# Kernel tuning notes

Hardware: AMD Instinct MI355X
Metric: run time of the kernel (lower is better)

Reference implementation:

```python
import jax, jax.numpy as jnp
import numpy as np

H = 16  # num_heads
LN_EPS = 1e-5


def setup_inputs() -> dict:
    key = jax.random.key(0)
    ks = jax.random.split(key, 16)
    B, L, E = 4, 1024, 1024
    x = jax.random.normal(ks[0], (B, L, E), dtype=jnp.float32)
    bias = jax.random.normal(ks[1], (B, H, L, L), dtype=jnp.float32)
    mask = jax.random.randint(ks[2], (B, L), 0, 2, dtype=jnp.int32)
    w = lambda k: jax.random.normal(k, (E, E), dtype=jnp.float32) * 0.02
    return {
        "x": x, "bias": bias, "mask": mask,
        "Wq": w(ks[3]), "bq": jnp.zeros((E,), jnp.float32),
        "Wk": w(ks[4]), "bk": jnp.zeros((E,), jnp.float32),
        "Wv": w(ks[5]), "bv": jnp.zeros((E,), jnp.float32),
        "Wo": w(ks[6]), "bo": jnp.zeros((E,), jnp.float32),
        "gamma": jnp.ones((E,), jnp.float32),
        "beta": jnp.zeros((E,), jnp.float32),
        "gate": jax.random.normal(ks[7], (H,), dtype=jnp.float32) * 0.1,
    }


def reference(x, bias, mask, Wq, bq, Wk, bk, Wv, bv, Wo, bo, gamma, beta, gate):
    B, L, E = x.shape
    D = E // H
    scale = 1.0 / jnp.sqrt(jnp.float32(D))
    residual = x
    # LayerNorm
    mu = jnp.mean(x, axis=-1, keepdims=True)
    var = jnp.mean(jnp.square(x - mu), axis=-1, keepdims=True)
    xn = (x - mu) * jax.lax.rsqrt(var + LN_EPS) * gamma + beta

    def proj(W, b):  # [B,L,E] -> [B,H,L,D]
        return (xn @ W.T + b).reshape(B, L, H, D).transpose(0, 2, 1, 3)

    Q, K, V = proj(Wq, bq), proj(Wk, bk), proj(Wv, bv)
    # logits = QK^T/sqrt(D) + alpha_h * bias   -> [B,H,L,L]
    logits = jnp.einsum("bhqd,bhkd->bhqk", Q, K) * scale
    logits = logits + gate[None, :, None, None] * bias
    mf = mask.astype(x.dtype)
    logits = logits + (1.0 - mf)[:, None, None, :] * -10000.0  # key mask
    attn = jax.nn.softmax(logits, axis=-1)
    attn = jnp.nan_to_num(attn) * mf[:, None, :, None]  # query mask
    out = jnp.einsum("bhqk,bhkd->bqhd", attn, V).reshape(B, L, E)
    out = out * mf[..., None]
    return residual + out @ Wo.T + bo
```

## Files before the change

### kernel.cpp

```cpp
#include <hip/hip_runtime.h>
#include <math.h>

typedef unsigned short u16;
typedef __attribute__((ext_vector_type(8))) short bf16x8;
typedef __attribute__((ext_vector_type(4))) float f32x4;

#define MFMA16(a, b, c) __builtin_amdgcn_mfma_f32_16x16x32_bf16(a, b, c, 0, 0, 0)

__device__ __forceinline__ void gld16(const void* g, void* l) {
  __builtin_amdgcn_global_load_lds((const __attribute__((address_space(1))) void*)g,
                                   (__attribute__((address_space(3))) void*)l, 16, 0, 0);
}

__device__ __forceinline__ u16 f2bf(float f) {
  unsigned u = __float_as_uint(f);
  u += 0x7fffu + ((u >> 16) & 1u);
  return (u16)(u >> 16);
}

__global__ __launch_bounds__(256) void k_castw(const float* __restrict__ wq, const float* __restrict__ wk,
                                               const float* __restrict__ wv, const float* __restrict__ wo,
                                               u16* __restrict__ dst) {
  int t = blockIdx.x * 256 + threadIdx.x;
  int which = t >> 18;
  int off = (t & 0x3ffff) << 2;
  const float* src = (which == 0) ? wq : (which == 1) ? wk : (which == 2) ? wv : wo;
  float4 v = *reinterpret_cast<const float4*>(src + off);
  ushort4 o;
  o.x = f2bf(v.x); o.y = f2bf(v.y); o.z = f2bf(v.z); o.w = f2bf(v.w);
  *reinterpret_cast<ushort4*>(dst + ((size_t)which << 20) + off) = o;
}

__global__ __launch_bounds__(256) void k_ln(const float* __restrict__ x, const float* __restrict__ gamma,
                                            const float* __restrict__ beta, u16* __restrict__ xn) {
  const int row = blockIdx.x, tid = threadIdx.x;
  const int lane = tid & 63, w = tid >> 6;
  const float* xr = x + (size_t)row * 1024;
  float4 v = *reinterpret_cast<const float4*>(xr + tid * 4);
  float s = v.x + v.y + v.z + v.w;
  float s2 = v.x * v.x + v.y * v.y + v.z * v.z + v.w * v.w;
  #pragma unroll
  for (int m = 1; m < 64; m <<= 1) { s += __shfl_xor(s, m); s2 += __shfl_xor(s2, m); }
  __shared__ float ps[4], pq[4];
  if (lane == 0) { ps[w] = s; pq[w] = s2; }
  __syncthreads();
  float S = ps[0] + ps[1] + ps[2] + ps[3];
  float S2 = pq[0] + pq[1] + pq[2] + pq[3];
  float mu = S * (1.f / 1024.f);
  float var = S2 * (1.f / 1024.f) - mu * mu;
  float rstd = rsqrtf(var + 1e-5f);
  float4 g = *reinterpret_cast<const float4*>(gamma + tid * 4);
  float4 bt = *reinterpret_cast<const float4*>(beta + tid * 4);
  ushort4 o;
  o.x = f2bf((v.x - mu) * rstd * g.x + bt.x);
  o.y = f2bf((v.y - mu) * rstd * g.y + bt.y);
  o.z = f2bf((v.z - mu) * rstd * g.z + bt.z);
  o.w = f2bf((v.w - mu) * rstd * g.w + bt.w);
  *reinterpret_cast<ushort4*>(xn + (size_t)row * 1024 + tid * 4) = o;
}

__global__ __launch_bounds__(256) void k_gemm_qkv(const u16* __restrict__ xn,
    const u16* __restrict__ wqb, const u16* __restrict__ wkb, const u16* __restrict__ wvb,
    const float* __restrict__ bq, const float* __restrict__ bk, const float* __restrict__ bv,
    u16* __restrict__ qo, u16* __restrict__ ko, u16* __restrict__ vo) {
  __shared__ __align__(16) u16 lA[128 * 32];
  __shared__ __align__(16) u16 lB[128 * 32];
  const int tid = threadIdx.x;
  const int w = tid >> 6, lane = tid & 63;
  const int wr = w >> 1, wc = w & 1;
  const int lane15 = lane & 15, lgrp = lane >> 4;
  const int m0 = blockIdx.y * 128, n0 = blockIdx.x * 128;
  const int z = blockIdx.z;
  const u16* Bt = (z == 0) ? wqb : (z == 1) ? wkb : wvb;

  f32x4 zero = {0.f, 0.f, 0.f, 0.f};
  f32x4 acc[4][4];
  #pragma unroll
  for (int i = 0; i < 4; i++)
    #pragma unroll
    for (int j = 0; j < 4; j++) acc[i][j] = zero;

  const int srow = w * 16 + (lane >> 2);
  const int scol = (lane & 3) * 8;
  for (int kt = 0; kt < 32; kt++) {
    const int k0 = kt * 32;
    #pragma unroll
    for (int c = 0; c < 2; c++) {
      gld16(xn + (size_t)(m0 + c * 64 + srow) * 1024 + k0 + scol, (char*)lA + c * 4096 + w * 1024);
      gld16(Bt + (size_t)(n0 + c * 64 + srow) * 1024 + k0 + scol, (char*)lB + c * 4096 + w * 1024);
    }
    __syncthreads();
    bf16x8 aF[4], bF[4];
    #pragma unroll
    for (int f = 0; f < 4; f++) {
      aF[f] = *reinterpret_cast<const bf16x8*>(&lA[(wr * 64 + f * 16 + lane15) * 32 + lgrp * 8]);
      bF[f] = *reinterpret_cast<const bf16x8*>(&lB[(wc * 64 + f * 16 + lane15) * 32 + lgrp * 8]);
    }
    #pragma unroll
    for (int fm = 0; fm < 4; fm++)
      #pragma unroll
      for (int fn = 0; fn < 4; fn++)
        acc[fm][fn] = MFMA16(aF[fm], bF[fn], acc[fm][fn]);
    __syncthreads();
  }

  const float* bvec = (z == 0) ? bq : (z == 1) ? bk : bv;
  u16* dst = (z == 0) ? qo : (z == 1) ? ko : vo;
  #pragma unroll
  for (int fm = 0; fm < 4; fm++)
    #pragma unroll
    for (int fn = 0; fn < 4; fn++) {
      const int n = n0 + wc * 64 + fn * 16 + lane15;
      const int h = n >> 6, d = n & 63;
      const float bn = bvec[n];
      #pragma unroll
      for (int j = 0; j < 4; j++) {
        const int m = m0 + wr * 64 + fm * 16 + lgrp * 4 + j;
        const int b = m >> 10, lq = m & 1023;
        dst[(((size_t)(b * 16 + h)) * 1024 + lq) * 64 + d] = f2bf(acc[fm][fn][j] + bn);
      }
    }
}

__global__ __launch_bounds__(256) void k_transpose_v(const u16* __restrict__ V, u16* __restrict__ Vt) {
  __shared__ u16 t[64][64];
  const int bh = blockIdx.y, l0 = blockIdx.x * 64;
  const int tid = threadIdx.x;
  const int r = tid >> 2, c0 = (tid & 3) * 16;
  const u16* src = V + ((size_t)bh * 1024 + l0 + r) * 64 + c0;
  __align__(16) u16 tmp[16];
  *reinterpret_cast<uint4*>(tmp) = *reinterpret_cast<const uint4*>(src);
  *reinterpret_cast<uint4*>(tmp + 8) = *reinterpret_cast<const uint4*>(src + 8);
  #pragma unroll
  for (int i = 0; i < 16; i++) t[c0 + i][r] = tmp[i];
  __syncthreads();
  __align__(16) u16 o[16];
  #pragma unroll
  for (int i = 0; i < 16; i++) o[i] = t[r][c0 + i];
  u16* dst = Vt + ((size_t)bh * 64 + r) * 1024 + l0 + c0;
  *reinterpret_cast<uint4*>(dst) = *reinterpret_cast<const uint4*>(o);
  *reinterpret_cast<uint4*>(dst + 8) = *reinterpret_cast<const uint4*>(o + 8);
}

__global__ __launch_bounds__(256) void k_attn(const u16* __restrict__ Q, const u16* __restrict__ K,
    const u16* __restrict__ Vt, const float* __restrict__ bias, const int* __restrict__ mask,
    const float* __restrict__ gate, u16* __restrict__ O) {
  __shared__ __align__(16) u16 lK[32 * 64];
  __shared__ __align__(16) u16 lV[64 * 32];
  __shared__ __align__(16) u16 lP[4 * 16 * 32];
  const int tid = threadIdx.x;
  const int w = tid >> 6, lane = tid & 63;
  const int lane15 = lane & 15, lgrp = lane >> 4;
  const int bh = blockIdx.y;
  const int b = bh >> 4, h = bh & 15;
  const int q0 = blockIdx.x * 64 + w * 16;
  const float gateh = gate[h];
  const int* mb = mask + b * 1024;
  const float* biasq = bias + ((size_t)bh << 20);

  bf16x8 qf[2];
  #pragma unroll
  for (int kk = 0; kk < 2; kk++)
    qf[kk] = *reinterpret_cast<const bf16x8*>(Q + ((size_t)bh * 1024 + q0 + lane15) * 64 + kk * 32 + lgrp * 8);

  f32x4 zero = {0.f, 0.f, 0.f, 0.f};
  float m_i[4], l_i[4];
  f32x4 accO[4];
  #pragma unroll
  for (int j = 0; j < 4; j++) { m_i[j] = -INFINITY; l_i[j] = 0.f; }
  #pragma unroll
  for (int f = 0; f < 4; f++) accO[f] = zero;

  const int krow = tid >> 3, kcol = (tid & 7) * 8;
  const int vrow = tid >> 2, vcol = (tid & 3) * 8;
  const size_t kbase = (size_t)bh * 1024 * 64;
  const size_t vbase = (size_t)bh * 64 * 1024;

  for (int kb = 0; kb < 1024; kb += 32) {
    gld16(K + kbase + (size_t)(kb + krow) * 64 + kcol, (char*)lK + w * 1024);
    gld16(Vt + vbase + (size_t)vrow * 1024 + kb + vcol, (char*)lV + w * 1024);
    __syncthreads();

    f32x4 s[2];
    #pragma unroll
    for (int fn = 0; fn < 2; fn++) {
      bf16x8 kf0 = *reinterpret_cast<const bf16x8*>(&lK[(fn * 16 + lane15) * 64 + lgrp * 8]);
      bf16x8 kf1 = *reinterpret_cast<const bf16x8*>(&lK[(fn * 16 + lane15) * 64 + 32 + lgrp * 8]);
      s[fn] = MFMA16(qf[0], kf0, zero);
      s[fn] = MFMA16(qf[1], kf1, s[fn]);
    }
    int mk[2];
    float pmax[4] = {-INFINITY, -INFINITY, -INFINITY, -INFINITY};
    #pragma unroll
    for (int fn = 0; fn < 2; fn++) {
      const int kg = kb + fn * 16 + lane15;
      mk[fn] = mb[kg];
      #pragma unroll
      for (int j = 0; j < 4; j++) {
        const int qg = q0 + lgrp * 4 + j;
        float lg = s[fn][j] * 0.125f + gateh * biasq[(size_t)qg * 1024 + kg];
        lg = mk[fn] ? lg : -INFINITY;
        s[fn][j] = lg;
        pmax[j] = fmaxf(pmax[j], lg);
      }
    }
    #pragma unroll
    for (int j = 0; j < 4; j++)
      #pragma unroll
      for (int xm = 1; xm < 16; xm <<= 1)
        pmax[j] = fmaxf(pmax[j], __shfl_xor(pmax[j], xm));

    float corr[4], mnew[4], rs[4];
    #pragma unroll
    for (int j = 0; j < 4; j++) {
      mnew[j] = fmaxf(m_i[j], pmax[j]);
      corr[j] = (m_i[j] == -INFINITY) ? 0.f : __expf(m_i[j] - mnew[j]);
      rs[j] = 0.f;
    }
    #pragma unroll
    for (int fn = 0; fn < 2; fn++)
      #pragma unroll
      for (int j = 0; j < 4; j++) {
        float p = mk[fn] ? __expf(s[fn][j] - mnew[j]) : 0.f;
        rs[j] += p;
        lP[w * 512 + (lgrp * 4 + j) * 32 + fn * 16 + lane15] = f2bf(p);
      }
    #pragma unroll
    for (int j = 0; j < 4; j++) {
      #pragma unroll
      for (int xm = 1; xm < 16; xm <<= 1) rs[j] += __shfl_xor(rs[j], xm);
      l_i[j] = l_i[j] * corr[j] + rs[j];
      m_i[j] = mnew[j];
    }
    #pragma unroll
    for (int f = 0; f < 4; f++)
      #pragma unroll
      for (int j = 0; j < 4; j++) accO[f][j] *= corr[j];

    bf16x8 pf = *reinterpret_cast<const bf16x8*>(&lP[w * 512 + lane15 * 32 + lgrp * 8]);
    #pragma unroll
    for (int f = 0; f < 4; f++) {
      bf16x8 vf = *reinterpret_cast<const bf16x8*>(&lV[(f * 16 + lane15) * 32 + lgrp * 8]);
      accO[f] = MFMA16(pf, vf, accO[f]);
    }
    __syncthreads();
  }

  #pragma unroll
  for (int j = 0; j < 4; j++) {
    const int lq = q0 + lgrp * 4 + j;
    const float inv = (l_i[j] > 0.f) ? 1.f / l_i[j] : 0.f;
    const float mfq = mb[lq] ? 1.f : 0.f;
    #pragma unroll
    for (int f = 0; f < 4; f++) {
      const int d = f * 16 + lane15;
      O[(((size_t)(b * 1024 + lq)) * 16 + h) * 64 + d] = f2bf(accO[f][j] * inv * mfq);
    }
  }
}

__global__ __launch_bounds__(256) void k_gemm_out(const u16* __restrict__ A, const u16* __restrict__ Bt,
    const float* __restrict__ bo, const float* __restrict__ x, float* __restrict__ out) {
  __shared__ __align__(16) u16 lA[128 * 32];
  __shared__ __align__(16) u16 lB[128 * 32];
  const int tid = threadIdx.x;
  const int w = tid >> 6, lane = tid & 63;
  const int wr = w >> 1, wc = w & 1;
  const int lane15 = lane & 15, lgrp = lane >> 4;
  const int m0 = blockIdx.y * 128, n0 = blockIdx.x * 128;

  f32x4 zero = {0.f, 0.f, 0.f, 0.f};
  f32x4 acc[4][4];
  #pragma unroll
  for (int i = 0; i < 4; i++)
    #pragma unroll
    for (int j = 0; j < 4; j++) acc[i][j] = zero;

  const int srow = w * 16 + (lane >> 2);
  const int scol = (lane & 3) * 8;
  for (int kt = 0; kt < 32; kt++) {
    const int k0 = kt * 32;
    #pragma unroll
    for (int c = 0; c < 2; c++) {
      gld16(A + (size_t)(m0 + c * 64 + srow) * 1024 + k0 + scol, (char*)lA + c * 4096 + w * 1024);
      gld16(Bt + (size_t)(n0 + c * 64 + srow) * 1024 + k0 + scol, (char*)lB + c * 4096 + w * 1024);
    }
    __syncthreads();
    bf16x8 aF[4], bF[4];
    #pragma unroll
    for (int f = 0; f < 4; f++) {
      aF[f] = *reinterpret_cast<const bf16x8*>(&lA[(wr * 64 + f * 16 + lane15) * 32 + lgrp * 8]);
      bF[f] = *reinterpret_cast<const bf16x8*>(&lB[(wc * 64 + f * 16 + lane15) * 32 + lgrp * 8]);
    }
    #pragma unroll
    for (int fm = 0; fm < 4; fm++)
      #pragma unroll
      for (int fn = 0; fn < 4; fn++)
        acc[fm][fn] = MFMA16(aF[fm], bF[fn], acc[fm][fn]);
    __syncthreads();
  }

  #pragma unroll
  for (int fm = 0; fm < 4; fm++)
    #pragma unroll
    for (int fn = 0; fn < 4; fn++) {
      const int n = n0 + wc * 64 + fn * 16 + lane15;
      const float bn = bo[n];
      #pragma unroll
      for (int j = 0; j < 4; j++) {
        const int m = m0 + wr * 64 + fm * 16 + lgrp * 4 + j;
        out[(size_t)m * 1024 + n] = acc[fm][fn][j] + bn + x[(size_t)m * 1024 + n];
      }
    }
}

extern "C" void kernel_launch(void* const* d_in, const int* in_sizes, int n_in,
                              void* d_out, int out_size, void* d_ws, size_t ws_size,
                              hipStream_t stream) {
  const float* x     = (const float*)d_in[0];
  const float* bias  = (const float*)d_in[1];
  const int*   mask  = (const int*)d_in[2];
  const float* Wq    = (const float*)d_in[3];
  const float* bq    = (const float*)d_in[4];
  const float* Wk    = (const float*)d_in[5];
  const float* bk    = (const float*)d_in[6];
  const float* Wv    = (const float*)d_in[7];
  const float* bv    = (const float*)d_in[8];
  const float* Wo    = (const float*)d_in[9];
  const float* bo    = (const float*)d_in[10];
  const float* gamma = (const float*)d_in[11];
  const float* beta  = (const float*)d_in[12];
  const float* gate  = (const float*)d_in[13];
  float* out = (float*)d_out;

  u16* wsu  = (u16*)d_ws;
  u16* wqb  = wsu;
  u16* wkb  = wqb  + (1u << 20);
  u16* wvb  = wkb  + (1u << 20);
  u16* wob  = wvb  + (1u << 20);
  u16* xnb  = wob  + (1u << 20);
  u16* qb   = xnb  + (4u << 20);
  u16* kbuf = qb   + (4u << 20);
  u16* vb   = kbuf + (4u << 20);
  u16* vtb  = vb   + (4u << 20);
  u16* ob   = vtb  + (4u << 20);

  k_castw<<<4096, 256, 0, stream>>>(Wq, Wk, Wv, Wo, wqb);
  k_ln<<<4096, 256, 0, stream>>>(x, gamma, beta, xnb);
  k_gemm_qkv<<<dim3(8, 32, 3), 256, 0, stream>>>(xnb, wqb, wkb, wvb, bq, bk, bv, qb, kbuf, vb);
  k_transpose_v<<<dim3(16, 64), 256, 0, stream>>>(vb, vtb);
  k_attn<<<dim3(16, 64), 256, 0, stream>>>(qb, kbuf, vtb, bias, mask, gate, ob);
  k_gemm_out<<<dim3(8, 32), 256, 0, stream>>>(ob, wob, bo, x, out);
}
```

Baseline: 578.4 us.

## Restructure attention kernel: double-buffered 64-key tiles, transposed MFMA, swizzled LDS

Rewrites the flash-attention kernel to process 64 keys per iteration with double-buffered K/V tiles in LDS, prefetching the next tile while computing the current one. Operands are swapped in the MFMAs so each lane owns one query row. That makes softmax reductions need only two cross-lane shuffles, and bias and mask are read as float4/int4 vectors along the key dimension. LDS reads use an XOR swizzle to avoid bank conflicts, and the output is stored as packed vectors. The key mask now adds -10000 instead of forcing -inf, matching the reference. This uses more LDS per block, which may lower occupancy.

```diff
diff --git a/kernel.cpp b/kernel.cpp
--- a/kernel.cpp
+++ b/kernel.cpp
@@ -145,117 +145,128 @@
 __global__ __launch_bounds__(256) void k_attn(const u16* __restrict__ Q, const u16* __restrict__ K,
     const u16* __restrict__ Vt, const float* __restrict__ bias, const int* __restrict__ mask,
     const float* __restrict__ gate, u16* __restrict__ O) {
-  __shared__ __align__(16) u16 lK[32 * 64];
-  __shared__ __align__(16) u16 lV[64 * 32];
-  __shared__ __align__(16) u16 lP[4 * 16 * 32];
+  __shared__ __align__(16) u16 lK[2][4096];
+  __shared__ __align__(16) u16 lV[2][4096];
+  __shared__ __align__(16) u16 lP[4][16 * 72];
   const int tid = threadIdx.x;
   const int w = tid >> 6, lane = tid & 63;
-  const int lane15 = lane & 15, lgrp = lane >> 4;
+  const int l15 = lane & 15, lg4 = lane >> 4;
   const int bh = blockIdx.y;
   const int b = bh >> 4, h = bh & 15;
-  const int q0 = blockIdx.x * 64 + w * 16;
+  const int qg = blockIdx.x * 64 + w * 16 + l15;
   const float gateh = gate[h];
   const int* mb = mask + b * 1024;
-  const float* biasq = bias + ((size_t)bh << 20);
-
-  bf16x8 qf[2];
-  #pragma unroll
-  for (int kk = 0; kk < 2; kk++)
-    qf[kk] = *reinterpret_cast<const bf16x8*>(Q + ((size_t)bh * 1024 + q0 + lane15) * 64 + kk * 32 + lgrp * 8);
+  const float* biasr = bias + ((size_t)bh << 20) + (size_t)qg * 1024;
+  const size_t kvbase = (size_t)bh * 65536;
+
+  bf16x8 qf0 = *reinterpret_cast<const bf16x8*>(Q + kvbase + (size_t)qg * 64 + lg4 * 8);
+  bf16x8 qf1 = *reinterpret_cast<const bf16x8*>(Q + kvbase + (size_t)qg * 64 + 32 + lg4 * 8);
 
   f32x4 zero = {0.f, 0.f, 0.f, 0.f};
-  float m_i[4], l_i[4];
+  float m_i = -INFINITY, l_i = 0.f;
   f32x4 accO[4];
   #pragma unroll
-  for (int j = 0; j < 4; j++) { m_i[j] = -INFINITY; l_i[j] = 0.f; }
-  #pragma unroll
   for (int f = 0; f < 4; f++) accO[f] = zero;
 
-  const int krow = tid >> 3, kcol = (tid & 7) * 8;
-  const int vrow = tid >> 2, vcol = (tid & 3) * 8;
-  const size_t kbase = (size_t)bh * 1024 * 64;
-  const size_t vbase = (size_t)bh * 64 * 1024;
-
-  for (int kb = 0; kb < 1024; kb += 32) {
-    gld16(K + kbase + (size_t)(kb + krow) * 64 + kcol, (char*)lK + w * 1024);
-    gld16(Vt + vbase + (size_t)vrow * 1024 + kb + vcol, (char*)lV + w * 1024);
-    __syncthreads();
-
-    f32x4 s[2];
-    #pragma unroll
-    for (int fn = 0; fn < 2; fn++) {
-      bf16x8 kf0 = *reinterpret_cast<const bf16x8*>(&lK[(fn * 16 + lane15) * 64 + lgrp * 8]);
-      bf16x8 kf1 = *reinterpret_cast<const bf16x8*>(&lK[(fn * 16 + lane15) * 64 + 32 + lgrp * 8]);
-      s[fn] = MFMA16(qf[0], kf0, zero);
-      s[fn] = MFMA16(qf[1], kf1, s[fn]);
-    }
-    int mk[2];
-    float pmax[4] = {-INFINITY, -INFINITY, -INFINITY, -INFINITY};
-    #pragma unroll
-    for (int fn = 0; fn < 2; fn++) {
-      const int kg = kb + fn * 16 + lane15;
-      mk[fn] = mb[kg];
+  const int srow = w * 8 + (lane >> 3);
+  const int scol = ((lane & 7) ^ (lane >> 3)) * 8;
+  const int ldst = w * 1024;
+  const int swz = (l15 & 7) << 4;
+
+  #pragma unroll
+  for (int c = 0; c < 2; c++) {
+    gld16(K + kvbase + (size_t)(c * 32 + srow) * 64 + scol, (char*)lK[0] + c * 4096 + ldst);
+    gld16(Vt + kvbase + (size_t)(c * 32 + srow) * 1024 + scol, (char*)lV[0] + c * 4096 + ldst);
+  }
+  __syncthreads();
+
+  int cur = 0;
+  for (int t = 0; t < 16; t++) {
+    const int kb = t * 64;
+    if (t < 15) {
+      const int kb2 = kb + 64;
+      #pragma unroll
+      for (int c = 0; c < 2; c++) {
+        gld16(K + kvbase + (size_t)(kb2 + c * 32 + srow) * 64 + scol, (char*)lK[cur ^ 1] + c * 4096 + ldst);
+        gld16(Vt + kvbase + (size_t)(c * 32 + srow) * 1024 + kb2 + scol, (char*)lV[cur ^ 1] + c * 4096 + ldst);
+      }
+    }
+
+    const char* lkb = (const char*)lK[cur];
+    f32x4 s[4];
+    #pragma unroll
+    for (int fn = 0; fn < 4; fn++) {
+      const char* rowp = lkb + (fn * 16 + l15) * 128;
+      bf16x8 kf0 = *reinterpret_cast<const bf16x8*>(rowp + ((lg4 * 16) ^ swz));
+      bf16x8 kf1 = *reinterpret_cast<const bf16x8*>(rowp + ((64 + lg4 * 16) ^ swz));
+      s[fn] = MFMA16(kf0, qf0, zero);
+      s[fn] = MFMA16(kf1, qf1, s[fn]);
+    }
+
+    float p[16];
+    float pmax = -INFINITY;
+    #pragma unroll
+    for (int fn = 0; fn < 4; fn++) {
+      const int kg = kb + fn * 16 + lg4 * 4;
+      float4 b4 = *reinterpret_cast<const float4*>(biasr + kg);
+      int4 m4 = *reinterpret_cast<const int4*>(mb + kg);
       #pragma unroll
       for (int j = 0; j < 4; j++) {
-        const int qg = q0 + lgrp * 4 + j;
-        float lg = s[fn][j] * 0.125f + gateh * biasq[(size_t)qg * 1024 + kg];
-        lg = mk[fn] ? lg : -INFINITY;
-        s[fn][j] = lg;
-        pmax[j] = fmaxf(pmax[j], lg);
+        const float bj = (j == 0) ? b4.x : (j == 1) ? b4.y : (j == 2) ? b4.z : b4.w;
+        const int mj = (j == 0) ? m4.x : (j == 1) ? m4.y : (j == 2) ? m4.z : m4.w;
+        float lgt = s[fn][j] * 0.125f + gateh * bj + (mj ? 0.f : -10000.f);
+        p[fn * 4 + j] = lgt;
+        pmax = fmaxf(pmax, lgt);
       }
     }
-    #pragma unroll
-    for (int j = 0; j < 4; j++)
-      #pragma unroll
-      for (int xm = 1; xm < 16; xm <<= 1)
-        pmax[j] = fmaxf(pmax[j], __shfl_xor(pmax[j], xm));
-
-    float corr[4], mnew[4], rs[4];
-    #pragma unroll
-    for (int j = 0; j < 4; j++) {
-      mnew[j] = fmaxf(m_i[j], pmax[j]);
-      corr[j] = (m_i[j] == -INFINITY) ? 0.f : __expf(m_i[j] - mnew[j]);
-      rs[j] = 0.f;
-    }
-    #pragma unroll
-    for (int fn = 0; fn < 2; fn++)
-      #pragma unroll
-      for (int j = 0; j < 4; j++) {
-        float p = mk[fn] ? __expf(s[fn][j] - mnew[j]) : 0.f;
-        rs[j] += p;
-        lP[w * 512 + (lgrp * 4 + j) * 32 + fn * 16 + lane15] = f2bf(p);
-      }
-    #pragma unroll
-    for (int j = 0; j < 4; j++) {
-      #pragma unroll
-      for (int xm = 1; xm < 16; xm <<= 1) rs[j] += __shfl_xor(rs[j], xm);
-      l_i[j] = l_i[j] * corr[j] + rs[j];
-      m_i[j] = mnew[j];
-    }
+    pmax = fmaxf(pmax, __shfl_xor(pmax, 16));
+    pmax = fmaxf(pmax, __shfl_xor(pmax, 32));
+    const float mnew = fmaxf(m_i, pmax);
+    const float corr = __expf(m_i - mnew);
+    float rs = 0.f;
+    #pragma unroll
+    for (int i = 0; i < 16; i++) { p[i] = __expf(p[i] - mnew); rs += p[i]; }
+    rs += __shfl_xor(rs, 16);
+    rs += __shfl_xor(rs, 32);
+    l_i = l_i * corr + rs;
+    m_i = mnew;
     #pragma unroll
     for (int f = 0; f < 4; f++)
       #pragma unroll
-      for (int j = 0; j < 4; j++) accO[f][j] *= corr[j];
-
-    bf16x8 pf = *reinterpret_cast<const bf16x8*>(&lP[w * 512 + lane15 * 32 + lgrp * 8]);
+      for (int j = 0; j < 4; j++) accO[f][j] *= corr;
+
+    u16* lpw = lP[w];
+    #pragma unroll
+    for (int fn = 0; fn < 4; fn++) {
+      ushort4 pk;
+      pk.x = f2bf(p[fn * 4 + 0]); pk.y = f2bf(p[fn * 4 + 1]);
+      pk.z = f2bf(p[fn * 4 + 2]); pk.w = f2bf(p[fn * 4 + 3]);
+      *reinterpret_cast<ushort4*>(lpw + l15 * 72 + fn * 16 + lg4 * 4) = pk;
+    }
+
+    bf16x8 pf0 = *reinterpret_cast<const bf16x8*>((const char*)lpw + l15 * 144 + lg4 * 16);
+    bf16x8 pf1 = *reinterpret_cast<const bf16x8*>((const char*)lpw + l15 * 144 + 64 + lg4 * 16);
+    const char* lvb = (const char*)lV[cur];
     #pragma unroll
     for (int f = 0; f < 4; f++) {
-      bf16x8 vf = *reinterpret_cast<const bf16x8*>(&lV[(f * 16 + lane15) * 32 + lgrp * 8]);
-      accO[f] = MFMA16(pf, vf, accO[f]);
-    }
-    __syncthreads();
-  }
-
-  #pragma unroll
-  for (int j = 0; j < 4; j++) {
-    const int lq = q0 + lgrp * 4 + j;
-    const float inv = (l_i[j] > 0.f) ? 1.f / l_i[j] : 0.f;
-    const float mfq = mb[lq] ? 1.f : 0.f;
-    #pragma unroll
-    for (int f = 0; f < 4; f++) {
-      const int d = f * 16 + lane15;
-      O[(((size_t)(b * 1024 + lq)) * 16 + h) * 64 + d] = f2bf(accO[f][j] * inv * mfq);
-    }
+      const char* rowp = lvb + (f * 16 + l15) * 128;
+      bf16x8 vf0 = *reinterpret_cast<const bf16x8*>(rowp + ((lg4 * 16) ^ swz));
+      bf16x8 vf1 = *reinterpret_cast<const bf16x8*>(rowp + ((64 + lg4 * 16) ^ swz));
+      accO[f] = MFMA16(vf0, pf0, accO[f]);
+      accO[f] = MFMA16(vf1, pf1, accO[f]);
+    }
+    __syncthreads();
+    cur ^= 1;
+  }
+
+  const float sc = (mb[qg] ? 1.f : 0.f) / l_i;
+  u16* orow = O + (((size_t)(b * 1024 + qg)) * 16 + h) * 64;
+  #pragma unroll
+  for (int f = 0; f < 4; f++) {
+    ushort4 o4;
+    o4.x = f2bf(accO[f][0] * sc); o4.y = f2bf(accO[f][1] * sc);
+    o4.z = f2bf(accO[f][2] * sc); o4.w = f2bf(accO[f][3] * sc);
+    *reinterpret_cast<ushort4*>(orow + f * 16 + lg4 * 4) = o4;
   }
 }
 
```

Result: faster. 542.0 us (-6.3%).
